# Performance work log

Measured on AMD Instinct MI355X. Metric: run time of the kernel, lower is better.

## Reference

```python
import jax, jax.numpy as jnp
import numpy as np

# dims: batch, seq, d_model, mlp_width, num_experts, lora_rank
B, S, D, M, E, R = 4, 1024, 2048, 5632, 8, 16
LORA_ALPHA = 32
SCALING = LORA_ALPHA / R  # = 2.0


def setup_inputs() -> dict:
    key = jax.random.key(0)
    ks = jax.random.split(key, 13)
    s = 0.02
    f32 = jnp.float32
    return {
        'x':  jax.random.normal(ks[0], (B, S, D), f32),
        # router: nn.Linear(d_model, num_experts)
        'Wr': jax.random.normal(ks[1], (E, D), f32) * s,
        'br': jax.random.normal(ks[2], (E,), f32) * s,
        # frozen original MLP weights (torch Linear layout [out, in])
        'Wg': jax.random.normal(ks[3], (M, D), f32) * s,
        'Wu': jax.random.normal(ks[4], (M, D), f32) * s,
        'Wd': jax.random.normal(ks[5], (D, M), f32) * s,
        # shared LoRA A matrices [rank, fan_in]
        'Ag': jax.random.normal(ks[6], (R, D), f32) * s,
        'Au': jax.random.normal(ks[7], (R, D), f32) * s,
        'Ad': jax.random.normal(ks[8], (R, M), f32) * s,
        # per-expert LoRA B matrices [E, fan_out, rank] (zero-init in the
        # original; randomized here so gradients/outputs are non-trivial)
        'Bg': jax.random.normal(ks[9], (E, M, R), f32) * s,
        'Bu': jax.random.normal(ks[10], (E, M, R), f32) * s,
        'Bd': jax.random.normal(ks[11], (E, D, R), f32) * s,
    }


def _lora_moe_dense(x, W, A, Bexp, routing):
    """Dense MoE LoRA: original_proj(x) + sum_e routing[...,e] * (x @ A^T @ B_e^T) * scaling.
    x: [b,s,in], W: [out,in], A: [r,in], Bexp: [E,out,r], routing: [b,s,E].
    Identical math to stacking all experts then weighted-summing, but the
    shared A lets us weight the tiny [b,s,E,r] hidden instead of [b,s,E,out].
    """
    orig = jnp.einsum('bsi,oi->bso', x, W)
    h = jnp.einsum('bsi,ri->bsr', x, A)            # shared low-rank hidden
    hw = jnp.einsum('bsr,bse->bser', h, routing)   # routing-weighted hidden
    lora = jnp.einsum('bser,eor->bso', hw, Bexp) * SCALING
    return orig + lora


def reference(x, Wr, br, Wg, Wu, Wd, Ag, Au, Ad, Bg, Bu, Bd):
    logits = jnp.einsum('bsd,ed->bse', x, Wr) + br
    routing = jax.nn.softmax(logits, axis=-1)
    idx = jnp.argmax(routing, axis=-1)
    y_hard = jax.nn.one_hot(idx, E, dtype=logits.dtype)
    # straight-through expert choice
    expert_choice = y_hard - jax.lax.stop_gradient(routing) + routing
    gate = _lora_moe_dense(x, Wg, Ag, Bg, routing)
    up = _lora_moe_dense(x, Wu, Au, Bu, routing)
    h = jax.nn.silu(gate) * up  # LLaMA-style SwiGLU act_fn
    out = _lora_moe_dense(h, Wd, Ad, Bd, routing)
    return out, routing, expert_choice
```

## Files before the change

kernel.cpp:

```cpp
#include <hip/hip_runtime.h>

#define DEV __device__ __forceinline__

typedef unsigned short u16;
typedef __bf16 bf16x8 __attribute__((ext_vector_type(8)));
typedef float f32x4 __attribute__((ext_vector_type(4)));

static DEV u16 f2bf(float f) {
    union { float f; unsigned u; } v; v.f = f;
    unsigned r = v.u + 0x7fffu + ((v.u >> 16) & 1u);
    return (u16)(r >> 16);
}
static DEV float bf2f(u16 u) {
    union { unsigned u; float f; } v; v.u = ((unsigned)u) << 16;
    return v.f;
}
static DEV void g2l16(const u16* g, u16* l) {
    __builtin_amdgcn_global_load_lds(
        (const __attribute__((address_space(1))) void*)g,
        (__attribute__((address_space(3))) void*)l, 16, 0, 0);
}

#define BAR()    do { __builtin_amdgcn_s_barrier(); __builtin_amdgcn_sched_barrier(0); } while (0)
#define WAITV(N) asm volatile("s_waitcnt vmcnt(" #N ")" ::: "memory")

#define MM16(A, B, FMO, FNO) do {                                            \
    __builtin_amdgcn_s_setprio(1);                                           \
    _Pragma("unroll")                                                        \
    for (int fm_ = 0; fm_ < 4; ++fm_)                                        \
      _Pragma("unroll")                                                      \
      for (int fn_ = 0; fn_ < 2; ++fn_)                                      \
        _Pragma("unroll")                                                    \
        for (int ks_ = 0; ks_ < 2; ++ks_)                                    \
          acc[(FMO) + fm_][(FNO) + fn_] = __builtin_amdgcn_mfma_f32_16x16x32_bf16( \
              A[fm_][ks_], B[fn_][ks_], acc[(FMO) + fm_][(FNO) + fn_], 0, 0, 0); \
    __builtin_amdgcn_s_setprio(0);                                           \
} while (0)


__global__ __launch_bounds__(256) void k_conv(
    const float* __restrict__ Wg, const float* __restrict__ Wu, const float* __restrict__ Wd,
    const float* __restrict__ Bg, const float* __restrict__ Bu, const float* __restrict__ Bd,
    u16* __restrict__ Wg16, u16* __restrict__ Wu16, u16* __restrict__ Wd16,
    u16* __restrict__ Bgx, u16* __restrict__ Bux, u16* __restrict__ Bdx)
{
    const long long NW = 2883584;
    const long long NB = 180224;
    const long long ND = 65536;
    long long gid = (long long)blockIdx.x * 256 + threadIdx.x;
    if (gid < 3 * NW) {
        const float* s; u16* d; long long g = gid;
        if (g < NW)           { s = Wg; d = Wg16; }
        else if (g < 2 * NW)  { s = Wu; d = Wu16; g -= NW; }
        else                  { s = Wd; d = Wd16; g -= 2 * NW; }
        float4 v = *(const float4*)(s + g * 4);
        ushort4 o; o.x = f2bf(v.x); o.y = f2bf(v.y); o.z = f2bf(v.z); o.w = f2bf(v.w);
        *(ushort4*)(d + g * 4) = o;
    } else {
        long long g = gid - 3 * NW;
        const float* s; u16* d; int nr;
        if (g < NB)               { s = Bg; d = Bgx; nr = 5632; }
        else if (g < 2 * NB)      { s = Bu; d = Bux; nr = 5632; g -= NB; }
        else if (g < 2 * NB + ND) { s = Bd; d = Bdx; nr = 2048; g -= 2 * NB; }
        else return;
        int n = (int)(g >> 5);
        int j0 = ((int)g & 31) * 4;
        int e = j0 >> 4, r0 = j0 & 15;
        float4 v = *(const float4*)&s[((size_t)e * nr + n) * 16 + r0];
        ushort4 o; o.x = f2bf(v.x); o.y = f2bf(v.y); o.z = f2bf(v.z); o.w = f2bf(v.w);
        *(ushort4*)&d[(size_t)n * 128 + j0] = o;
    }
}

__global__ __launch_bounds__(256) void k_router(
    const float* __restrict__ x, const float* __restrict__ Wr,
    const float* __restrict__ Ag, const float* __restrict__ Au,
    u16* __restrict__ x16, float* __restrict__ fin1)
{
    __shared__ float xs[64][65];
    __shared__ float wsm[40][64];
    const int rb = blockIdx.x, ksp = blockIdx.y;
    const int row0 = rb * 64;
    const int t = threadIdx.x;
    const int rloc = t & 63, og = t >> 6;
    float acc[10];
#pragma unroll
    for (int o = 0; o < 10; ++o) acc[o] = 0.f;

    for (int c4 = 0; c4 < 4; ++c4) {
        const int k0 = ksp * 256 + c4 * 64;
        __syncthreads();
#pragma unroll
        for (int i = 0; i < 4; ++i) {
            int idx = t + i * 256;
            int r = idx >> 4, c = (idx & 15) * 4;
            float4 v = *(const float4*)&x[(size_t)(row0 + r) * 2048 + k0 + c];
            xs[r][c + 0] = v.x; xs[r][c + 1] = v.y; xs[r][c + 2] = v.z; xs[r][c + 3] = v.w;
            ushort4 o; o.x = f2bf(v.x); o.y = f2bf(v.y); o.z = f2bf(v.z); o.w = f2bf(v.w);
            *(ushort4*)&x16[(size_t)(row0 + r) * 2048 + k0 + c] = o;
        }
#pragma unroll
        for (int i = 0; i < 3; ++i) {
            int idx = t + i * 256;
            if (idx < 640) {
                int r = idx >> 4, c = (idx & 15) * 4;
                const float* src = (r < 8) ? (Wr + (size_t)r * 2048)
                                : (r < 24) ? (Ag + (size_t)(r - 8) * 2048)
                                           : (Au + (size_t)(r - 24) * 2048);
                float4 v = *(const float4*)&src[k0 + c];
                wsm[r][c + 0] = v.x; wsm[r][c + 1] = v.y; wsm[r][c + 2] = v.z; wsm[r][c + 3] = v.w;
            }
        }
        __syncthreads();
#pragma unroll
        for (int k = 0; k < 64; ++k) {
            float xv = xs[rloc][k];
#pragma unroll
            for (int o = 0; o < 10; ++o) acc[o] += xv * wsm[og * 10 + o][k];
        }
    }
    float* dst = fin1 + ((size_t)ksp * 4096 + row0 + rloc) * 40 + og * 10;
#pragma unroll
    for (int o = 0; o < 10; ++o) dst[o] = acc[o];
}

__global__ __launch_bounds__(256) void k_fin1(
    const float* __restrict__ fin1, const float* __restrict__ br,
    float* __restrict__ routing_ws, float* __restrict__ out_rt, float* __restrict__ out_ec,
    u16* __restrict__ hwg, u16* __restrict__ hwu)
{
    const int row = blockIdx.x * 256 + threadIdx.x;
    float s[40];
#pragma unroll
    for (int j = 0; j < 40; ++j) s[j] = 0.f;
    for (int p = 0; p < 8; ++p) {
        const float* src = fin1 + ((size_t)p * 4096 + row) * 40;
#pragma unroll
        for (int j = 0; j < 40; ++j) s[j] += src[j];
    }
    float lg[8]; float m = -1e30f;
#pragma unroll
    for (int e = 0; e < 8; ++e) { lg[e] = s[e] + br[e]; m = fmaxf(m, lg[e]); }
    float ex[8]; float sum = 0.f;
#pragma unroll
    for (int e = 0; e < 8; ++e) { ex[e] = expf(lg[e] - m); sum += ex[e]; }
    float r8[8];
#pragma unroll
    for (int e = 0; e < 8; ++e) r8[e] = ex[e] / sum;
    int best = 0;
#pragma unroll
    for (int e = 1; e < 8; ++e) if (r8[e] > r8[best]) best = e;
#pragma unroll
    for (int e = 0; e < 8; ++e) {
        routing_ws[(size_t)row * 8 + e] = r8[e];
        out_rt[(size_t)row * 8 + e] = r8[e];
        float yh = (e == best) ? 1.f : 0.f;
        out_ec[(size_t)row * 8 + e] = (yh - r8[e]) + r8[e];
    }
#pragma unroll
    for (int e = 0; e < 8; ++e) {
        float re = r8[e];
#pragma unroll
        for (int rk = 0; rk < 16; ++rk) {
            hwg[(size_t)row * 128 + e * 16 + rk] = f2bf(2.f * s[8 + rk] * re);
            hwu[(size_t)row * 128 + e * 16 + rk] = f2bf(2.f * s[24 + rk] * re);
        }
    }
}

template<int MODE>
__global__ __launch_bounds__(512, 2) void k_gemm8(
    const u16* __restrict__ A0, int lda0,
    const u16* __restrict__ A1g, const u16* __restrict__ A1u,
    const u16* __restrict__ B0g, int ldb0, const u16* __restrict__ B0u,
    const u16* __restrict__ B1g, const u16* __restrict__ B1u,
    int Ksplit,
    float* __restrict__ outF0, float* __restrict__ outF1,
    u16* __restrict__ outHg, u16* __restrict__ outHu,
    int nbm, int nbn)
{
    __shared__ u16 lds[65536];
    const int t = threadIdx.x;
    const int nwg = (int)gridDim.x;
    const int orig = (int)blockIdx.x;
    const int sw = (orig & 7) * (nwg >> 3) + (orig >> 3);
    const int bm = sw % nbm; const int rest = sw / nbm;
    const int bn = rest % nbn; const int z = rest / nbn;

    const int row0 = bm * 256, col0 = bn * 256;
    int ktb, ntl;
    if (MODE == 0) { ktb = z ? 46 : 0; ntl = z ? 44 : 46; }
    else           { ktb = 0;          ntl = 34; }
    const int kend = ktb + ntl;
    const u16* A1 = (MODE == 1 && z) ? A1u : A1g;
    const u16* B0 = (MODE == 1 && z) ? B0u : B0g;
    const u16* B1 = (MODE == 1 && z) ? B1u : B1g;

    const int lane = t & 63, lr = lane & 15, lg = lane >> 4;
    const int wid = t >> 6, wr = wid >> 2, wcol = wid & 3;
    const int arow = wr * 128 + lr;
    const int brow = wcol * 64 + lr;
    const int sa = (arow & 7) << 3;
    const int sb = (brow & 7) << 3;

    auto stg = [&](int kt, int h, int isB) {
        const int k0 = kt * 64;
        const u16* s; int ld; int kc;
        if (isB) { if (k0 >= Ksplit) { s = B1; ld = 128; kc = k0 - Ksplit; } else { s = B0; ld = ldb0; kc = k0; } }
        else     { if (k0 >= Ksplit) { s = A1; ld = 128; kc = k0 - Ksplit; } else { s = A0; ld = lda0; kc = k0; } }
        const int r0 = isB ? col0 : row0;
        u16* base = lds + (isB ? 32768 : 0) + (kt & 1) * 16384;
#pragma unroll
        for (int j = 0; j < 2; ++j) {
            const int o = h * 16384 + j * 8192 + t * 16;
            const int r = o >> 7;
            const int cb = (o & 127) ^ ((r & 7) << 4);
            g2l16(s + (size_t)(r0 + r) * ld + kc + (cb >> 1), (u16*)((char*)base + o));
        }
    };
    auto rdA = [&](int buf, int fb, bf16x8 a[4][2]) {
#pragma unroll
        for (int fm = 0; fm < 4; ++fm)
#pragma unroll
            for (int ks = 0; ks < 2; ++ks)
                a[fm][ks] = *(const bf16x8*)&lds[buf * 16384 + (arow + (fb + fm) * 16) * 64
                                                 + (((ks << 5) | (lg << 3)) ^ sa)];
    };
    auto rdB = [&](int buf, int fb, bf16x8 b[2][2]) {
#pragma unroll
        for (int fn = 0; fn < 2; ++fn)
#pragma unroll
            for (int ks = 0; ks < 2; ++ks)
                b[fn][ks] = *(const bf16x8*)&lds[32768 + buf * 16384 + (brow + (fb + fn) * 16) * 64
                                                 + (((ks << 5) | (lg << 3)) ^ sb)];
    };

    f32x4 acc[8][4];
    const f32x4 zf = {0.f, 0.f, 0.f, 0.f};
#pragma unroll
    for (int i = 0; i < 8; ++i)
#pragma unroll
        for (int j = 0; j < 4; ++j) acc[i][j] = zf;

    stg(ktb, 0, 0); stg(ktb, 1, 0);
    stg(ktb, 0, 1); stg(ktb, 1, 1);
    stg(ktb + 1, 0, 1); stg(ktb + 1, 1, 1);
    WAITV(4);
    BAR();

    const int ni = ntl >> 1;
    for (int i = 0; i < ni; ++i) {
        const int kt0 = ktb + 2 * i, kt1 = kt0 + 1;
        const bool s2 = (kt0 + 2 < kend), s3 = (kt1 + 2 < kend);
        bf16x8 alo[4][2], ahi[4][2], b01[2][2], b23[2][2];
        rdA(0, 0, alo); rdB(0, 0, b01);
        stg(kt1, 0, 0);
        BAR(); MM16(alo, b01, 0, 0); BAR();
        rdB(0, 2, b23);
        stg(kt1, 1, 0);
        BAR(); MM16(alo, b23, 0, 2); BAR();
        rdA(0, 4, ahi);
        if (s2) stg(kt0 + 2, 0, 1);
        BAR(); MM16(ahi, b01, 4, 0); BAR();
        if (s2) { stg(kt0 + 2, 1, 1); WAITV(4); } else { WAITV(0); }
        BAR(); MM16(ahi, b23, 4, 2); BAR();
        rdA(1, 0, alo); rdB(1, 0, b01);
        if (s2) stg(kt0 + 2, 0, 0);
        BAR(); MM16(alo, b01, 0, 0); BAR();
        rdB(1, 2, b23);
        if (s2) stg(kt0 + 2, 1, 0);
        BAR(); MM16(alo, b23, 0, 2); BAR();
        rdA(1, 4, ahi);
        if (s3) stg(kt1 + 2, 0, 1);
        BAR(); MM16(ahi, b01, 4, 0); BAR();
        if (s3) { stg(kt1 + 2, 1, 1); WAITV(4); } else { WAITV(0); }
        BAR(); MM16(ahi, b23, 4, 2); BAR();
    }

#pragma unroll
    for (int fm = 0; fm < 8; ++fm) {
#pragma unroll
        for (int fn = 0; fn < 4; ++fn) {
            const int r = row0 + wr * 128 + fm * 16 + lg * 4;
            const int c = col0 + wcol * 64 + fn * 16 + lr;
            f32x4 v = acc[fm][fn];
            if constexpr (MODE == 0) {
                float* out = z ? outF1 : outF0;
#pragma unroll
                for (int j = 0; j < 4; ++j) out[(size_t)(r + j) * 2048 + c] = v[j];
            } else {
                u16* out = z ? outHu : outHg;
#pragma unroll
                for (int j = 0; j < 4; ++j) out[(size_t)(r + j) * 5632 + c] = f2bf(v[j]);
            }
        }
    }
}

__global__ __launch_bounds__(256) void k_hd(
    u16* __restrict__ g, const u16* __restrict__ u,
    const float* __restrict__ Ad, float* __restrict__ fin2)
{
    __shared__ float hs[64][65];
    __shared__ float as2[16][64];
    const int rb = blockIdx.x, ksp = blockIdx.y;
    const int row0 = rb * 64;
    const int t = threadIdx.x;
    const int rloc = t & 63, og = t >> 6;
    float acc[4] = {0.f, 0.f, 0.f, 0.f};
    for (int c4 = 0; c4 < 11; ++c4) {
        const int k0 = ksp * 704 + c4 * 64;
        __syncthreads();
#pragma unroll
        for (int i = 0; i < 4; ++i) {
            int idx = t + i * 256;
            int r = idx >> 4, cc = (idx & 15) * 4;
            size_t go = (size_t)(row0 + r) * 5632 + k0 + cc;
            ushort4 gv = *(const ushort4*)&g[go];
            ushort4 uv = *(const ushort4*)&u[go];
            float h0, h1, h2, h3;
            { float gg = bf2f(gv.x); h0 = gg / (1.f + __expf(-gg)) * bf2f(uv.x); }
            { float gg = bf2f(gv.y); h1 = gg / (1.f + __expf(-gg)) * bf2f(uv.y); }
            { float gg = bf2f(gv.z); h2 = gg / (1.f + __expf(-gg)) * bf2f(uv.z); }
            { float gg = bf2f(gv.w); h3 = gg / (1.f + __expf(-gg)) * bf2f(uv.w); }
            hs[r][cc + 0] = h0; hs[r][cc + 1] = h1; hs[r][cc + 2] = h2; hs[r][cc + 3] = h3;
            ushort4 hv; hv.x = f2bf(h0); hv.y = f2bf(h1); hv.z = f2bf(h2); hv.w = f2bf(h3);
            *(ushort4*)&g[go] = hv;
        }
        {
            int r = t >> 4, cc = (t & 15) * 4;
            float4 w = *(const float4*)&Ad[(size_t)r * 5632 + k0 + cc];
            as2[r][cc + 0] = w.x; as2[r][cc + 1] = w.y; as2[r][cc + 2] = w.z; as2[r][cc + 3] = w.w;
        }
        __syncthreads();
#pragma unroll
        for (int k = 0; k < 64; ++k) {
            float hv = hs[rloc][k];
#pragma unroll
            for (int o = 0; o < 4; ++o) acc[o] += hv * as2[og * 4 + o][k];
        }
    }
    float* dst = fin2 + ((size_t)ksp * 4096 + row0 + rloc) * 16 + og * 4;
#pragma unroll
    for (int o = 0; o < 4; ++o) dst[o] = acc[o];
}

__global__ __launch_bounds__(256) void k_fin2(
    const float* __restrict__ fin2, const float* __restrict__ routing_ws, u16* __restrict__ hwd)
{
    const int row = blockIdx.x * 256 + threadIdx.x;
    float hd[16];
#pragma unroll
    for (int j = 0; j < 16; ++j) hd[j] = 0.f;
    for (int p = 0; p < 8; ++p) {
        const float* src = fin2 + ((size_t)p * 4096 + row) * 16;
#pragma unroll
        for (int j = 0; j < 16; ++j) hd[j] += src[j];
    }
#pragma unroll
    for (int e = 0; e < 8; ++e) {
        float re = routing_ws[(size_t)row * 8 + e];
#pragma unroll
        for (int rk = 0; rk < 16; ++rk)
            hwd[(size_t)row * 128 + e * 16 + rk] = f2bf(2.f * hd[rk] * re);
    }
}

__global__ __launch_bounds__(256) void k_reduce(
    float* __restrict__ o, const float* __restrict__ p1)
{
    size_t i = ((size_t)blockIdx.x * 256 + threadIdx.x) * 4;
    float4 a = *(const float4*)&o[i];
    float4 b = *(const float4*)&p1[i];
    float4 r; r.x = a.x + b.x; r.y = a.y + b.y; r.z = a.z + b.z; r.w = a.w + b.w;
    *(float4*)&o[i] = r;
}

extern "C" void kernel_launch(void* const* d_in, const int* in_sizes, int n_in,
                              void* d_out, int out_size, void* d_ws, size_t ws_size,
                              hipStream_t stream)
{
    (void)in_sizes; (void)n_in; (void)out_size; (void)ws_size;
    const float* x  = (const float*)d_in[0];
    const float* Wr = (const float*)d_in[1];
    const float* br = (const float*)d_in[2];
    const float* Wg = (const float*)d_in[3];
    const float* Wu = (const float*)d_in[4];
    const float* Wd = (const float*)d_in[5];
    const float* Ag = (const float*)d_in[6];
    const float* Au = (const float*)d_in[7];
    const float* Ad = (const float*)d_in[8];
    const float* Bg = (const float*)d_in[9];
    const float* Bu = (const float*)d_in[10];
    const float* Bd = (const float*)d_in[11];

    float* outp   = (float*)d_out;
    float* out_rt = outp + 8388608;
    float* out_ec = out_rt + 32768;

    char* p = (char*)d_ws;
    auto carve = [&](size_t n) -> char* { char* r = p; p += (n + 255) & ~(size_t)255; return r; };
    u16*   x16        = (u16*)carve(16777216);
    u16*   hwg        = (u16*)carve(1048576);
    u16*   hwu        = (u16*)carve(1048576);
    u16*   hwd        = (u16*)carve(1048576);
    float* routing_ws = (float*)carve(131072);
    float* fin1       = (float*)carve(5242880);
    float* fin2       = (float*)carve(2097152);
    u16*   Wg16       = (u16*)carve(23068672);
    u16*   Wu16       = (u16*)carve(23068672);
    u16*   Wd16       = (u16*)carve(23068672);
    u16*   Bgx        = (u16*)carve(1441792);
    u16*   Bux        = (u16*)carve(1441792);
    u16*   Bdx        = (u16*)carve(524288);
    u16*   gbuf       = (u16*)carve(46137344);
    u16*   ubuf       = (u16*)carve(46137344);
    float* part1      = (float*)ubuf;

    k_conv<<<dim3(35456), dim3(256), 0, stream>>>(Wg, Wu, Wd, Bg, Bu, Bd,
                                                  Wg16, Wu16, Wd16, Bgx, Bux, Bdx);
    k_router<<<dim3(64, 8), dim3(256), 0, stream>>>(x, Wr, Ag, Au, x16, fin1);
    k_fin1<<<dim3(16), dim3(256), 0, stream>>>(fin1, br, routing_ws, out_rt, out_ec, hwg, hwu);
    k_gemm8<1><<<dim3(704), dim3(512), 0, stream>>>(
        x16, 2048, hwg, hwu, Wg16, 2048, Wu16, Bgx, Bux,
        2048, (float*)nullptr, (float*)nullptr, gbuf, ubuf, 16, 22);
    k_hd<<<dim3(64, 8), dim3(256), 0, stream>>>(gbuf, ubuf, Ad, fin2);
    k_fin2<<<dim3(16), dim3(256), 0, stream>>>(fin2, routing_ws, hwd);
    k_gemm8<0><<<dim3(256), dim3(512), 0, stream>>>(
        gbuf, 5632, hwd, hwd, Wd16, 5632, Wd16, Bdx, Bdx,
        5632, outp, part1, (u16*)nullptr, (u16*)nullptr, 16, 8);
    k_reduce<<<dim3(8192), dim3(256), 0, stream>>>(outp, part1);
}
```

Baseline: 472.5 us.

## Overlap LDS fragment reads with MFMA and use incremental global pointers

```diff
diff --git a/kernel.cpp b/kernel.cpp
--- a/kernel.cpp
+++ b/kernel.cpp
@@ -192,6 +192,7 @@
     if (MODE == 0) { ktb = z ? 46 : 0; ntl = z ? 44 : 46; }
     else           { ktb = 0;          ntl = 34; }
     const int kend = ktb + ntl;
+    const int swT = Ksplit >> 6;
     const u16* A1 = (MODE == 1 && z) ? A1u : A1g;
     const u16* B0 = (MODE == 1 && z) ? B0u : B0g;
     const u16* B1 = (MODE == 1 && z) ? B1u : B1g;
@@ -203,35 +204,41 @@
     const int sa = (arow & 7) << 3;
     const int sb = (brow & 7) << 3;
 
-    auto stg = [&](int kt, int h, int isB) {
-        const int k0 = kt * 64;
-        const u16* s; int ld; int kc;
-        if (isB) { if (k0 >= Ksplit) { s = B1; ld = 128; kc = k0 - Ksplit; } else { s = B0; ld = ldb0; kc = k0; } }
-        else     { if (k0 >= Ksplit) { s = A1; ld = 128; kc = k0 - Ksplit; } else { s = A0; ld = lda0; kc = k0; } }
-        const int r0 = isB ? col0 : row0;
-        u16* base = lds + (isB ? 32768 : 0) + (kt & 1) * 16384;
-#pragma unroll
-        for (int j = 0; j < 2; ++j) {
-            const int o = h * 16384 + j * 8192 + t * 16;
-            const int r = o >> 7;
-            const int cb = (o & 127) ^ ((r & 7) << 4);
-            g2l16(s + (size_t)(r0 + r) * ld + kc + (cb >> 1), (u16*)((char*)base + o));
-        }
+    const int r00 = t >> 3;
+    const int c00 = ((t & 7) * 8) ^ ((r00 & 7) << 3);
+    const u16* pA = A0 + (size_t)(row0 + r00) * lda0 + ktb * 64 + c00;
+    const u16* pB = B0 + (size_t)(col0 + r00) * ldb0 + ktb * 64 + c00;
+    int dA1 = lda0 * 64, dA2 = lda0 * 128;
+    int dB1 = ldb0 * 64, dB2 = ldb0 * 128;
+
+    auto stgA = [&](int kt, int h, int bufu) {
+        if (kt == swT && h == 0) { pA = A1 + (size_t)(row0 + r00) * 128 + c00; dA1 = 8192; dA2 = 16384; }
+        const u16* b = pA + h * dA2;
+        g2l16(b,       &lds[bufu + h * 8192 + t * 8]);
+        g2l16(b + dA1, &lds[bufu + h * 8192 + 4096 + t * 8]);
+        if (h) pA += 64;
     };
-    auto rdA = [&](int buf, int fb, bf16x8 a[4][2]) {
+    auto stgB = [&](int kt, int h, int bufu) {
+        if (kt == swT && h == 0) { pB = B1 + (size_t)(col0 + r00) * 128 + c00; dB1 = 8192; dB2 = 16384; }
+        const u16* b = pB + h * dB2;
+        g2l16(b,       &lds[32768 + bufu + h * 8192 + t * 8]);
+        g2l16(b + dB1, &lds[32768 + bufu + h * 8192 + 4096 + t * 8]);
+        if (h) pB += 64;
+    };
+    auto rdA = [&](int bufu, int fb, bf16x8 (&d)[4][2]) {
 #pragma unroll
         for (int fm = 0; fm < 4; ++fm)
 #pragma unroll
             for (int ks = 0; ks < 2; ++ks)
-                a[fm][ks] = *(const bf16x8*)&lds[buf * 16384 + (arow + (fb + fm) * 16) * 64
+                d[fm][ks] = *(const bf16x8*)&lds[bufu + (arow + (fb + fm) * 16) * 64
                                                  + (((ks << 5) | (lg << 3)) ^ sa)];
     };
-    auto rdB = [&](int buf, int fb, bf16x8 b[2][2]) {
+    auto rdB = [&](int bufu, int fb, bf16x8 (&d)[2][2]) {
 #pragma unroll
         for (int fn = 0; fn < 2; ++fn)
 #pragma unroll
             for (int ks = 0; ks < 2; ++ks)
-                b[fn][ks] = *(const bf16x8*)&lds[32768 + buf * 16384 + (brow + (fb + fn) * 16) * 64
+                d[fn][ks] = *(const bf16x8*)&lds[32768 + bufu + (brow + (fb + fn) * 16) * 64
                                                  + (((ks << 5) | (lg << 3)) ^ sb)];
     };
 
@@ -242,39 +249,57 @@
 #pragma unroll
         for (int j = 0; j < 4; ++j) acc[i][j] = zf;
 
-    stg(ktb, 0, 0); stg(ktb, 1, 0);
-    stg(ktb, 0, 1); stg(ktb, 1, 1);
-    stg(ktb + 1, 0, 1); stg(ktb + 1, 1, 1);
+    bf16x8 va[4][2], vah[4][2], vb0[2][2], vb1[2][2];
+
+    stgA(ktb, 0, 0); stgA(ktb, 1, 0);
+    stgB(ktb, 0, 0); stgB(ktb, 1, 0);
+    stgB(ktb + 1, 0, 16384); stgB(ktb + 1, 1, 16384);
     WAITV(4);
     BAR();
+    rdA(0, 0, va); rdB(0, 0, vb0);
 
     const int ni = ntl >> 1;
     for (int i = 0; i < ni; ++i) {
         const int kt0 = ktb + 2 * i, kt1 = kt0 + 1;
         const bool s2 = (kt0 + 2 < kend), s3 = (kt1 + 2 < kend);
-        bf16x8 alo[4][2], ahi[4][2], b01[2][2], b23[2][2];
-        rdA(0, 0, alo); rdB(0, 0, b01);
-        stg(kt1, 0, 0);
-        BAR(); MM16(alo, b01, 0, 0); BAR();
-        rdB(0, 2, b23);
-        stg(kt1, 1, 0);
-        BAR(); MM16(alo, b23, 0, 2); BAR();
-        rdA(0, 4, ahi);
-        if (s2) stg(kt0 + 2, 0, 1);
-        BAR(); MM16(ahi, b01, 4, 0); BAR();
-        if (s2) { stg(kt0 + 2, 1, 1); WAITV(4); } else { WAITV(0); }
-        BAR(); MM16(ahi, b23, 4, 2); BAR();
-        rdA(1, 0, alo); rdB(1, 0, b01);
-        if (s2) stg(kt0 + 2, 0, 0);
-        BAR(); MM16(alo, b01, 0, 0); BAR();
-        rdB(1, 2, b23);
-        if (s2) stg(kt0 + 2, 1, 0);
-        BAR(); MM16(alo, b23, 0, 2); BAR();
-        rdA(1, 4, ahi);
-        if (s3) stg(kt1 + 2, 0, 1);
-        BAR(); MM16(ahi, b01, 4, 0); BAR();
-        if (s3) { stg(kt1 + 2, 1, 1); WAITV(4); } else { WAITV(0); }
-        BAR(); MM16(ahi, b23, 4, 2); BAR();
+        stgA(kt1, 0, 16384);
+        BAR();
+        rdB(0, 2, vb1);
+        MM16(va, vb0, 0, 0);
+        BAR();
+        stgA(kt1, 1, 16384);
+        BAR();
+        rdA(0, 4, vah);
+        MM16(va, vb1, 0, 2);
+        BAR();
+        if (s2) stgB(kt0 + 2, 0, 0);
+        BAR();
+        MM16(vah, vb0, 4, 0);
+        BAR();
+        if (s2) { stgB(kt0 + 2, 1, 0); WAITV(4); } else { WAITV(0); }
+        BAR();
+        rdA(16384, 0, va); rdB(16384, 0, vb0);
+        MM16(vah, vb1, 4, 2);
+        BAR();
+        if (s2) stgA(kt0 + 2, 0, 0);
+        BAR();
+        rdB(16384, 2, vb1);
+        MM16(va, vb0, 0, 0);
+        BAR();
+        if (s2) stgA(kt0 + 2, 1, 0);
+        BAR();
+        rdA(16384, 4, vah);
+        MM16(va, vb1, 0, 2);
+        BAR();
+        if (s3) stgB(kt1 + 2, 0, 16384);
+        BAR();
+        MM16(vah, vb0, 4, 0);
+        BAR();
+        if (s3) { stgB(kt1 + 2, 1, 16384); WAITV(4); } else { WAITV(0); }
+        BAR();
+        if (s2) { rdA(0, 0, va); rdB(0, 0, vb0); }
+        MM16(vah, vb1, 4, 2);
+        BAR();
     }
 
 #pragma unroll
```

Result: slower. 556.9 us (+17.9%).
